# Optimization experiments

Measured on AMD Instinct MI355X. Metric: run time of the kernel, lower is better.

## Reference

```python
import jax, jax.numpy as jnp
import numpy as np

THRESH_FACTOR = 0.7


def ternarize(w):
    # w: [in_features, out_features]; per-row (dim 0) delta/alpha stats
    n = w.shape[1]
    abs_w = jnp.abs(w)
    delta = (THRESH_FACTOR / n) * abs_w.sum(axis=1, keepdims=True)  # [in, 1]
    mask = abs_w > delta
    count = mask.sum(axis=1, keepdims=True).astype(w.dtype)
    alpha = jnp.where(mask, abs_w, 0).sum(axis=1, keepdims=True) / count  # [in, 1]
    tern = jnp.where(w > delta, 1.0, jnp.where(w < -delta, -1.0, 0.0)).astype(w.dtype)
    return tern * alpha


def setup_inputs() -> dict:
    key = jax.random.key(0)
    k1, k2, k3 = jax.random.split(key, 3)
    B, IN, OUT = 8192, 4096, 4096
    x = jax.random.normal(k1, (B, IN), dtype=jnp.float32)
    # kaiming-uniform-ish then clamp to [-1, 1] as in the module
    bound_w = float(np.sqrt(6.0 / ((1.0 + 5.0) * IN)))
    weights = jax.random.uniform(k2, (IN, OUT), minval=-bound_w, maxval=bound_w, dtype=jnp.float32)
    weights = jnp.clip(weights, -1.0, 1.0)
    bound_b = 1.0 / float(np.sqrt(IN))
    bias = jax.random.uniform(k3, (OUT,), minval=-bound_b, maxval=bound_b, dtype=jnp.float32)
    return {"x": x, "weights": weights, "bias": bias}


def reference(x, weights, bias):
    w_t = ternarize(weights)
    return jnp.matmul(x, w_t) + bias
```

## Files before the change

### kernel.cpp

```cpp
#include <hip/hip_runtime.h>
#include <stdint.h>
#include <stddef.h>

#define IN_F 4096
#define OUT_F 4096

typedef int i32x4 __attribute__((ext_vector_type(4)));
typedef float f32x4 __attribute__((ext_vector_type(4)));


__device__ static inline void async16(const void* g, void* l) {
    __builtin_amdgcn_global_load_lds(
        (const __attribute__((address_space(1))) unsigned int*)g,
        (__attribute__((address_space(3))) unsigned int*)l,
        16, 0, 0);
}

__device__ static inline double wred_d(double v) {
#pragma unroll
    for (int o = 32; o > 0; o >>= 1) v += __shfl_down(v, o, 64);
    return v;
}

__device__ static inline int wred_i(int v) {
#pragma unroll
    for (int o = 32; o > 0; o >>= 1) v += __shfl_down(v, o, 64);
    return v;
}

__device__ static inline float wred_max(float v) {
#pragma unroll
    for (int o = 32; o > 0; o >>= 1) v = fmaxf(v, __shfl_down(v, o, 64));
    return v;
}


__global__ __launch_bounds__(256) void rowstats_tern_kernel(
    const float* __restrict__ w,
    float* __restrict__ alpha_o,
    int8_t* __restrict__ T) {
    __shared__ float rowbuf[OUT_F];
    __shared__ double sh_s[4], sh_m[4];
    __shared__ int sh_c[4];
    const int row = blockIdx.x;
    const int t = threadIdx.x;
    const int lane = t & 63, wv = t >> 6;
    const float4* wr = (const float4*)(w + (size_t)row * OUT_F);

    double s = 0.0;
#pragma unroll
    for (int it = 0; it < 4; ++it) {
        float4 v = wr[t + it * 256];
        ((float4*)rowbuf)[t + it * 256] = v;
        s += (double)fabsf(v.x) + (double)fabsf(v.y) +
             (double)fabsf(v.z) + (double)fabsf(v.w);
    }
    double sw = wred_d(s);
    if (lane == 0) sh_s[wv] = sw;
    __syncthreads();
    const double delta = (sh_s[0] + sh_s[1] + sh_s[2] + sh_s[3]) *
                         (0.7 / (double)OUT_F);

    int8_t* trow = T + (size_t)row * OUT_F;
    double ms = 0.0;
    int cnt = 0;
#pragma unroll
    for (int k = 0; k < 16; ++k) {
        float v = rowbuf[k * 256 + t];
        double a = (double)fabsf(v);
        if (a > delta) { ms += a; ++cnt; }
        int8_t q = 0;
        if ((double)v > delta)       q = 1;
        else if ((double)v < -delta) q = -1;
        trow[k * 256 + t] = q;
    }
    double msw = wred_d(ms);
    int cw = wred_i(cnt);
    if (lane == 0) { sh_m[wv] = msw; sh_c[wv] = cw; }
    __syncthreads();
    if (t == 0) {
        double mtot = sh_m[0] + sh_m[1] + sh_m[2] + sh_m[3];
        int ctot = sh_c[0] + sh_c[1] + sh_c[2] + sh_c[3];
        alpha_o[row] = (float)(mtot / (double)ctot);
    }
}


__global__ __launch_bounds__(256) void transpose_i8_kernel(
    const int8_t* __restrict__ T,
    int8_t* __restrict__ Tt) {
    __shared__ int8_t lds[64][72];
    const int t = threadIdx.x;
    const int i0 = blockIdx.y * 64;
    const int j0 = blockIdx.x * 64;

#pragma unroll
    for (int it = 0; it < 4; ++it) {
        int idx = it * 256 + t;
        int r = idx >> 4;
        int c4 = idx & 15;
        uchar4 v = *(const uchar4*)(T + (size_t)(i0 + r) * OUT_F + j0 + c4 * 4);
        lds[c4 * 4 + 0][r] = (int8_t)v.x;
        lds[c4 * 4 + 1][r] = (int8_t)v.y;
        lds[c4 * 4 + 2][r] = (int8_t)v.z;
        lds[c4 * 4 + 3][r] = (int8_t)v.w;
    }
    __syncthreads();
#pragma unroll
    for (int it = 0; it < 2; ++it) {
        int idx = it * 256 + t;
        int rr = idx >> 3;
        int cc = idx & 7;
        unsigned long long v = *(const unsigned long long*)&lds[rr][cc * 8];
        *(unsigned long long*)(Tt + (size_t)(j0 + rr) * IN_F + i0 + cc * 8) = v;
    }
}


__global__ __launch_bounds__(256) void xquant_kernel(
    const float* __restrict__ x,
    const float* __restrict__ alpha,
    int8_t* __restrict__ xq,
    float* __restrict__ scale_o) {
    __shared__ float rowbuf[IN_F];
    __shared__ float sh_mx[4];
    const int row = blockIdx.x;
    const int t = threadIdx.x;
    const int lane = t & 63, wv = t >> 6;
    const float4* xr = (const float4*)(x + (size_t)row * IN_F);
    const float4* ar = (const float4*)alpha;

    float mx = 0.0f;
#pragma unroll
    for (int it = 0; it < 4; ++it) {
        float4 v = xr[t + it * 256];
        float4 a = ar[t + it * 256];
        v.x *= a.x; v.y *= a.y; v.z *= a.z; v.w *= a.w;
        ((float4*)rowbuf)[t + it * 256] = v;
        mx = fmaxf(mx, fmaxf(fmaxf(fabsf(v.x), fabsf(v.y)),
                             fmaxf(fabsf(v.z), fabsf(v.w))));
    }
    float mw = wred_max(mx);
    if (lane == 0) sh_mx[wv] = mw;
    __syncthreads();
    const float rmax = fmaxf(fmaxf(sh_mx[0], sh_mx[1]), fmaxf(sh_mx[2], sh_mx[3]));
    const float inv = (rmax > 0.0f) ? (127.0f / rmax) : 0.0f;

    int8_t* qrow = xq + (size_t)row * IN_F;
#pragma unroll
    for (int k = 0; k < 16; ++k) {
        float v = rowbuf[k * 256 + t];
        qrow[k * 256 + t] = (int8_t)__float2int_rn(v * inv);
    }
    if (t == 0) scale_o[row] = (rmax > 0.0f) ? (rmax / 127.0f) : 1.0f;
}


#define GBARRIER() asm volatile("s_barrier" ::: "memory")

#define STAGE(G, GR0, TILE, LBASE, HALF)                                        \
    do {                                                                        \
        _Pragma("unroll")                                                       \
        for (int rr_ = 0; rr_ < 2; ++rr_) {                                     \
            const int L_ = (HALF) * 1024 + rr_ * 512 + t;                       \
            const int row_ = L_ >> 3;                                           \
            const int gch_ = (L_ & 7) ^ (row_ & 7);                             \
            async16((G) + (size_t)((GR0) + row_) * IN_F + (TILE) * 128 +        \
                        (gch_ << 4),                                            \
                    (LBASE) + (L_ << 4));                                       \
        }                                                                       \
    } while (0)

#define READ_A(BUF, MI0)                                                        \
    _Pragma("unroll")                                                           \
    for (int mi_ = 0; mi_ < 4; ++mi_) {                                         \
        a[2 * mi_]     = *(const i32x4*)((BUF) + offA_k0 + ((MI0) + mi_) * 2048); \
        a[2 * mi_ + 1] = *(const i32x4*)((BUF) + offA_k1 + ((MI0) + mi_) * 2048); \
    }

#define READ_B(BUF, NI0, DST)                                                   \
    _Pragma("unroll")                                                           \
    for (int ni_ = 0; ni_ < 2; ++ni_) {                                         \
        DST[2 * ni_]     = *(const i32x4*)((BUF) + offB_k0 + ((NI0) + ni_) * 2048); \
        DST[2 * ni_ + 1] = *(const i32x4*)((BUF) + offB_k1 + ((NI0) + ni_) * 2048); \
    }

#define MFMA_Q(MI0, NI0, BSRC)                                                  \
    do {                                                                        \
        __builtin_amdgcn_s_setprio(1);                                          \
        _Pragma("unroll")                                                       \
        for (int mi_ = 0; mi_ < 4; ++mi_) {                                     \
            _Pragma("unroll")                                                   \
            for (int ni_ = 0; ni_ < 2; ++ni_) {                                 \
                acc[(MI0) + mi_][(NI0) + ni_] =                                 \
                    __builtin_amdgcn_mfma_i32_16x16x64_i8(                      \
                        a[2 * mi_], BSRC[2 * ni_],                              \
                        acc[(MI0) + mi_][(NI0) + ni_], 0, 0, 0);                \
                acc[(MI0) + mi_][(NI0) + ni_] =                                 \
                    __builtin_amdgcn_mfma_i32_16x16x64_i8(                      \
                        a[2 * mi_ + 1], BSRC[2 * ni_ + 1],                      \
                        acc[(MI0) + mi_][(NI0) + ni_], 0, 0, 0);                \
            }                                                                   \
        }                                                                       \
        __builtin_amdgcn_s_setprio(0);                                          \
    } while (0)

__global__ __launch_bounds__(512, 2) void gemm_i8_8ph(
    const int8_t* __restrict__ Xq,
    const int8_t* __restrict__ Tq,
    const float* __restrict__ scale,
    const float* __restrict__ bias,
    float* __restrict__ out) {
    extern __shared__ __align__(16) int8_t lds[];
    const int K = IN_F;
    const int NT = K / 128;
    const int NI = NT / 2;

    const int t = threadIdx.x;
    const int lane = t & 63;
    const int wave = t >> 6;
    const int lm = lane & 15;
    const int qh = lane >> 4;
    const int wm = (wave >> 2) << 7;
    const int wn = (wave & 3) << 6;

    const int nwg = gridDim.x;
    const int id = blockIdx.x;
    const int swz = (id & 7) * (nwg >> 3) + (id >> 3);
    const int m0 = (swz >> 4) << 8;
    const int n0 = (swz & 15) << 8;

    int8_t* const A0  = lds;
    int8_t* const B0  = lds + 32768;
    int8_t* const A1b = lds + 65536;
    int8_t* const B1b = lds + 98304;

    const int swzs = lm & 7;
    const int offA_k0 = (wm + lm) * 128 + ((qh ^ swzs) << 4);
    const int offA_k1 = (wm + lm) * 128 + (((4 + qh) ^ swzs) << 4);
    const int offB_k0 = (wn + lm) * 128 + ((qh ^ swzs) << 4);
    const int offB_k1 = (wn + lm) * 128 + (((4 + qh) ^ swzs) << 4);

    i32x4 acc[8][4];
#pragma unroll
    for (int i = 0; i < 8; ++i)
#pragma unroll
        for (int j = 0; j < 4; ++j)
#pragma unroll
            for (int r = 0; r < 4; ++r) acc[i][j][r] = 0;

    i32x4 a[8], bA[4], bB[4];

    STAGE(Xq, m0, 0, A0, 0);
    STAGE(Xq, m0, 0, A0, 1);
    STAGE(Tq, n0, 0, B0, 0);
    STAGE(Tq, n0, 0, B0, 1);
    STAGE(Xq, m0, 1, A1b, 0);
    asm volatile("s_waitcnt vmcnt(2)" ::: "memory");
    GBARRIER();

#pragma unroll 1
    for (int i = 0; i < NI; ++i) {
        const int kt = 2 * i;
        READ_A(A0, 0);
        READ_B(B0, 0, bA);
        STAGE(Xq, m0, kt + 1, A1b, 1);
        GBARRIER();
        MFMA_Q(0, 0, bA);
        GBARRIER();
        READ_B(B0, 2, bB);
        STAGE(Tq, n0, kt + 1, B1b, 0);
        GBARRIER();
        MFMA_Q(0, 2, bB);
        GBARRIER();
        READ_A(A0, 4);
        STAGE(Tq, n0, kt + 1, B1b, 1);
        GBARRIER();
        MFMA_Q(4, 0, bA);
        GBARRIER();
        if (kt + 2 < NT) STAGE(Xq, m0, kt + 2, A0, 0);
        GBARRIER();
        MFMA_Q(4, 2, bB);
        if (i + 1 < NI) asm volatile("s_waitcnt vmcnt(2)" ::: "memory");
        else            asm volatile("s_waitcnt vmcnt(0)" ::: "memory");
        GBARRIER();
        READ_A(A1b, 0);
        READ_B(B1b, 0, bA);
        if (kt + 2 < NT) STAGE(Xq, m0, kt + 2, A0, 1);
        GBARRIER();
        MFMA_Q(0, 0, bA);
        GBARRIER();
        READ_B(B1b, 2, bB);
        if (kt + 2 < NT) STAGE(Tq, n0, kt + 2, B0, 0);
        GBARRIER();
        MFMA_Q(0, 2, bB);
        GBARRIER();
        READ_A(A1b, 4);
        if (kt + 2 < NT) STAGE(Tq, n0, kt + 2, B0, 1);
        GBARRIER();
        MFMA_Q(4, 0, bA);
        GBARRIER();
        if (kt + 3 < NT) STAGE(Xq, m0, kt + 3, A1b, 0);
        GBARRIER();
        MFMA_Q(4, 2, bB);
        if (i + 1 < NI) asm volatile("s_waitcnt vmcnt(2)" ::: "memory");
        GBARRIER();
    }

    const int q4 = qh << 2;
#pragma unroll
    for (int mi = 0; mi < 8; ++mi) {
        float sc[4];
#pragma unroll
        for (int r = 0; r < 4; ++r) sc[r] = scale[m0 + wm + mi * 16 + q4 + r];
#pragma unroll
        for (int ni = 0; ni < 4; ++ni) {
            int col = n0 + wn + ni * 16 + lm;
            float b = bias[col];
#pragma unroll
            for (int r = 0; r < 4; ++r) {
                int row = m0 + wm + mi * 16 + q4 + r;
                out[(size_t)row * OUT_F + col] =
                    (float)acc[mi][ni][r] * sc[r] + b;
            }
        }
    }
}


extern "C" void kernel_launch(void* const* d_in, const int* in_sizes, int n_in,
                              void* d_out, int out_size, void* d_ws, size_t ws_size,
                              hipStream_t stream) {
    const float* x = (const float*)d_in[0];
    const float* w = (const float*)d_in[1];
    const float* bias = (const float*)d_in[2];
    float* out = (float*)d_out;
    const int B = in_sizes[0] / IN_F;

    char* ws = (char*)d_ws;
    int8_t* Tt = (int8_t*)ws;
    int8_t* T = (int8_t*)(ws + (size_t)16777216);
    int8_t* Xq = (int8_t*)(ws + (size_t)16777216);
    float* alpha = (float*)(ws + (size_t)50331648);
    float* scale = (float*)(ws + (size_t)50331648 + 16384);

    static int lds_set = 0;
    if (!lds_set) {
        hipFuncSetAttribute((const void*)gemm_i8_8ph,
                            hipFuncAttributeMaxDynamicSharedMemorySize, 131072);
        lds_set = 1;
    }

    rowstats_tern_kernel<<<IN_F, 256, 0, stream>>>(w, alpha, T);
    transpose_i8_kernel<<<dim3(OUT_F / 64, IN_F / 64), 256, 0, stream>>>(T, Tt);
    xquant_kernel<<<B, 256, 0, stream>>>(x, alpha, Xq, scale);
    const int nwg = (B / 256) * (OUT_F / 256);
    gemm_i8_8ph<<<dim3(nwg), dim3(512), 131072, stream>>>(Xq, Tt, scale, bias, out);
}
```

Before: 384.9 us.

## Fuse ternarization into transpose, register-stage quantization, reorder GEMM prefetch

Row statistics now only compute alpha and delta, and ternarization moves into the transpose kernel, which reads fp32 weights directly and writes packed int8 transposed tiles. This removes the intermediate int8 weight matrix. The activation quantizer keeps each thread's 16 values in registers and writes one 16-byte packed store instead of staging through LDS. The GEMM main loop issues B-tile prefetches earlier and waits with a deeper vmcnt. The trade-off is that the weights are read twice, and delta shares a workspace slot with scale, which relies on kernel ordering.

```diff
diff --git a/kernel.cpp b/kernel.cpp
--- a/kernel.cpp
+++ b/kernel.cpp
@@ -6,7 +6,6 @@
 #define OUT_F 4096
 
 typedef int i32x4 __attribute__((ext_vector_type(4)));
-typedef float f32x4 __attribute__((ext_vector_type(4)));
 
 
 __device__ static inline void async16(const void* g, void* l) {
@@ -35,25 +34,24 @@
 }
 
 
-__global__ __launch_bounds__(256) void rowstats_tern_kernel(
+__global__ __launch_bounds__(256) void rowstats_kernel(
     const float* __restrict__ w,
     float* __restrict__ alpha_o,
-    int8_t* __restrict__ T) {
-    __shared__ float rowbuf[OUT_F];
+    double* __restrict__ delta_o) {
     __shared__ double sh_s[4], sh_m[4];
     __shared__ int sh_c[4];
     const int row = blockIdx.x;
     const int t = threadIdx.x;
     const int lane = t & 63, wv = t >> 6;
-    const float4* wr = (const float4*)(w + (size_t)row * OUT_F);
-
+    const float4* wr = (const float4*)(w + (size_t)row * OUT_F + t * 16);
+
+    float4 v[4];
     double s = 0.0;
 #pragma unroll
-    for (int it = 0; it < 4; ++it) {
-        float4 v = wr[t + it * 256];
-        ((float4*)rowbuf)[t + it * 256] = v;
-        s += (double)fabsf(v.x) + (double)fabsf(v.y) +
-             (double)fabsf(v.z) + (double)fabsf(v.w);
+    for (int i = 0; i < 4; ++i) {
+        v[i] = wr[i];
+        s += (double)fabsf(v[i].x) + (double)fabsf(v[i].y) +
+             (double)fabsf(v[i].z) + (double)fabsf(v[i].w);
     }
     double sw = wred_d(s);
     if (lane == 0) sh_s[wv] = sw;
@@ -61,18 +59,16 @@
     const double delta = (sh_s[0] + sh_s[1] + sh_s[2] + sh_s[3]) *
                          (0.7 / (double)OUT_F);
 
-    int8_t* trow = T + (size_t)row * OUT_F;
     double ms = 0.0;
     int cnt = 0;
 #pragma unroll
-    for (int k = 0; k < 16; ++k) {
-        float v = rowbuf[k * 256 + t];
-        double a = (double)fabsf(v);
-        if (a > delta) { ms += a; ++cnt; }
-        int8_t q = 0;
-        if ((double)v > delta)       q = 1;
-        else if ((double)v < -delta) q = -1;
-        trow[k * 256 + t] = q;
+    for (int i = 0; i < 4; ++i) {
+        float f[4] = {v[i].x, v[i].y, v[i].z, v[i].w};
+#pragma unroll
+        for (int j = 0; j < 4; ++j) {
+            double a = (double)fabsf(f[j]);
+            if (a > delta) { ms += a; ++cnt; }
+        }
     }
     double msw = wred_d(ms);
     int cw = wred_i(cnt);
@@ -82,37 +78,54 @@
         double mtot = sh_m[0] + sh_m[1] + sh_m[2] + sh_m[3];
         int ctot = sh_c[0] + sh_c[1] + sh_c[2] + sh_c[3];
         alpha_o[row] = (float)(mtot / (double)ctot);
-    }
-}
-
-
-__global__ __launch_bounds__(256) void transpose_i8_kernel(
-    const int8_t* __restrict__ T,
+        delta_o[row] = delta;
+    }
+}
+
+
+__global__ __launch_bounds__(256) void tern_transpose_kernel(
+    const float* __restrict__ w,
+    const double* __restrict__ delta_i,
     int8_t* __restrict__ Tt) {
-    __shared__ int8_t lds[64][72];
+    __shared__ unsigned int ldsb[128 * 33];
     const int t = threadIdx.x;
-    const int i0 = blockIdx.y * 64;
-    const int j0 = blockIdx.x * 64;
-
+    const int i0 = blockIdx.y * 128;
+    const int j0 = blockIdx.x * 128;
+
+#pragma unroll
+    for (int it = 0; it < 4; ++it) {
+        int bb = it * 256 + t;
+        int rg = bb >> 5;
+        int cc = bb & 31;
+        unsigned int col[4] = {0u, 0u, 0u, 0u};
+#pragma unroll
+        for (int k = 0; k < 4; ++k) {
+            int irow = i0 + rg * 4 + k;
+            float4 v = *(const float4*)(w + (size_t)irow * OUT_F + j0 + cc * 4);
+            double d = delta_i[irow];
+            float f[4] = {v.x, v.y, v.z, v.w};
+#pragma unroll
+            for (int j = 0; j < 4; ++j) {
+                int q = ((double)f[j] > d) ? 1 : (((double)f[j] < -d) ? -1 : 0);
+                col[j] |= (unsigned int)(q & 0xff) << (k * 8);
+            }
+        }
+#pragma unroll
+        for (int j = 0; j < 4; ++j)
+            ldsb[(cc * 4 + j) * 33 + rg] = col[j];
+    }
+    __syncthreads();
 #pragma unroll
     for (int it = 0; it < 4; ++it) {
         int idx = it * 256 + t;
-        int r = idx >> 4;
-        int c4 = idx & 15;
-        uchar4 v = *(const uchar4*)(T + (size_t)(i0 + r) * OUT_F + j0 + c4 * 4);
-        lds[c4 * 4 + 0][r] = (int8_t)v.x;
-        lds[c4 * 4 + 1][r] = (int8_t)v.y;
-        lds[c4 * 4 + 2][r] = (int8_t)v.z;
-        lds[c4 * 4 + 3][r] = (int8_t)v.w;
-    }
-    __syncthreads();
-#pragma unroll
-    for (int it = 0; it < 2; ++it) {
-        int idx = it * 256 + t;
         int rr = idx >> 3;
-        int cc = idx & 7;
-        unsigned long long v = *(const unsigned long long*)&lds[rr][cc * 8];
-        *(unsigned long long*)(Tt + (size_t)(j0 + rr) * IN_F + i0 + cc * 8) = v;
+        int c2 = idx & 7;
+        uint4 o;
+        o.x = ldsb[rr * 33 + c2 * 4 + 0];
+        o.y = ldsb[rr * 33 + c2 * 4 + 1];
+        o.z = ldsb[rr * 33 + c2 * 4 + 2];
+        o.w = ldsb[rr * 33 + c2 * 4 + 3];
+        *(uint4*)(Tt + (size_t)(j0 + rr) * IN_F + i0 + c2 * 16) = o;
     }
 }
 
@@ -122,21 +135,21 @@
     const float* __restrict__ alpha,
     int8_t* __restrict__ xq,
     float* __restrict__ scale_o) {
-    __shared__ float rowbuf[IN_F];
     __shared__ float sh_mx[4];
     const int row = blockIdx.x;
     const int t = threadIdx.x;
     const int lane = t & 63, wv = t >> 6;
-    const float4* xr = (const float4*)(x + (size_t)row * IN_F);
-    const float4* ar = (const float4*)alpha;
-
+    const float4* xr = (const float4*)(x + (size_t)row * IN_F + t * 16);
+    const float4* ar = (const float4*)(alpha + t * 16);
+
+    float4 xs[4];
     float mx = 0.0f;
 #pragma unroll
-    for (int it = 0; it < 4; ++it) {
-        float4 v = xr[t + it * 256];
-        float4 a = ar[t + it * 256];
+    for (int i = 0; i < 4; ++i) {
+        float4 v = xr[i];
+        float4 a = ar[i];
         v.x *= a.x; v.y *= a.y; v.z *= a.z; v.w *= a.w;
-        ((float4*)rowbuf)[t + it * 256] = v;
+        xs[i] = v;
         mx = fmaxf(mx, fmaxf(fmaxf(fabsf(v.x), fabsf(v.y)),
                              fmaxf(fabsf(v.z), fabsf(v.w))));
     }
@@ -146,12 +159,20 @@
     const float rmax = fmaxf(fmaxf(sh_mx[0], sh_mx[1]), fmaxf(sh_mx[2], sh_mx[3]));
     const float inv = (rmax > 0.0f) ? (127.0f / rmax) : 0.0f;
 
-    int8_t* qrow = xq + (size_t)row * IN_F;
-#pragma unroll
-    for (int k = 0; k < 16; ++k) {
-        float v = rowbuf[k * 256 + t];
-        qrow[k * 256 + t] = (int8_t)__float2int_rn(v * inv);
-    }
+    uint4 o;
+    unsigned int* op = (unsigned int*)&o;
+#pragma unroll
+    for (int i = 0; i < 4; ++i) {
+        float f[4] = {xs[i].x, xs[i].y, xs[i].z, xs[i].w};
+        unsigned int d = 0;
+#pragma unroll
+        for (int j = 0; j < 4; ++j) {
+            int q = __float2int_rn(f[j] * inv);
+            d |= (unsigned int)(q & 0xff) << (j * 8);
+        }
+        op[i] = d;
+    }
+    *(uint4*)(xq + (size_t)row * IN_F + t * 16) = o;
     if (t == 0) scale_o[row] = (rmax > 0.0f) ? (rmax / 127.0f) : 1.0f;
 }
 
@@ -255,8 +276,9 @@
     STAGE(Xq, m0, 0, A0, 1);
     STAGE(Tq, n0, 0, B0, 0);
     STAGE(Tq, n0, 0, B0, 1);
+    STAGE(Tq, n0, 1, B1b, 0);
     STAGE(Xq, m0, 1, A1b, 0);
-    asm volatile("s_waitcnt vmcnt(2)" ::: "memory");
+    asm volatile("s_waitcnt vmcnt(4)" ::: "memory");
     GBARRIER();
 
 #pragma unroll 1
@@ -264,46 +286,46 @@
         const int kt = 2 * i;
         READ_A(A0, 0);
         READ_B(B0, 0, bA);
+        STAGE(Tq, n0, kt + 1, B1b, 1);
+        GBARRIER();
+        MFMA_Q(0, 0, bA);
+        GBARRIER();
+        READ_B(B0, 2, bB);
         STAGE(Xq, m0, kt + 1, A1b, 1);
         GBARRIER();
-        MFMA_Q(0, 0, bA);
-        GBARRIER();
-        READ_B(B0, 2, bB);
-        STAGE(Tq, n0, kt + 1, B1b, 0);
-        GBARRIER();
         MFMA_Q(0, 2, bB);
         GBARRIER();
         READ_A(A0, 4);
-        STAGE(Tq, n0, kt + 1, B1b, 1);
+        if (kt + 2 < NT) STAGE(Tq, n0, kt + 2, B0, 0);
         GBARRIER();
         MFMA_Q(4, 0, bA);
         GBARRIER();
         if (kt + 2 < NT) STAGE(Xq, m0, kt + 2, A0, 0);
         GBARRIER();
         MFMA_Q(4, 2, bB);
-        if (i + 1 < NI) asm volatile("s_waitcnt vmcnt(2)" ::: "memory");
+        if (i + 1 < NI) asm volatile("s_waitcnt vmcnt(4)" ::: "memory");
         else            asm volatile("s_waitcnt vmcnt(0)" ::: "memory");
         GBARRIER();
         READ_A(A1b, 0);
         READ_B(B1b, 0, bA);
+        if (kt + 2 < NT) STAGE(Tq, n0, kt + 2, B0, 1);
+        GBARRIER();
+        MFMA_Q(0, 0, bA);
+        GBARRIER();
+        READ_B(B1b, 2, bB);
         if (kt + 2 < NT) STAGE(Xq, m0, kt + 2, A0, 1);
         GBARRIER();
-        MFMA_Q(0, 0, bA);
-        GBARRIER();
-        READ_B(B1b, 2, bB);
-        if (kt + 2 < NT) STAGE(Tq, n0, kt + 2, B0, 0);
-        GBARRIER();
         MFMA_Q(0, 2, bB);
         GBARRIER();
         READ_A(A1b, 4);
-        if (kt + 2 < NT) STAGE(Tq, n0, kt + 2, B0, 1);
+        if (kt + 3 < NT) STAGE(Tq, n0, kt + 3, B1b, 0);
         GBARRIER();
         MFMA_Q(4, 0, bA);
         GBARRIER();
         if (kt + 3 < NT) STAGE(Xq, m0, kt + 3, A1b, 0);
         GBARRIER();
         MFMA_Q(4, 2, bB);
-        if (i + 1 < NI) asm volatile("s_waitcnt vmcnt(2)" ::: "memory");
+        if (i + 1 < NI) asm volatile("s_waitcnt vmcnt(4)" ::: "memory");
         GBARRIER();
     }
 
@@ -339,9 +361,9 @@
 
     char* ws = (char*)d_ws;
     int8_t* Tt = (int8_t*)ws;
-    int8_t* T = (int8_t*)(ws + (size_t)16777216);
     int8_t* Xq = (int8_t*)(ws + (size_t)16777216);
     float* alpha = (float*)(ws + (size_t)50331648);
+    double* delta = (double*)(ws + (size_t)50331648 + 16384);
     float* scale = (float*)(ws + (size_t)50331648 + 16384);
 
     static int lds_set = 0;
@@ -351,8 +373,8 @@
         lds_set = 1;
     }
 
-    rowstats_tern_kernel<<<IN_F, 256, 0, stream>>>(w, alpha, T);
-    transpose_i8_kernel<<<dim3(OUT_F / 64, IN_F / 64), 256, 0, stream>>>(T, Tt);
+    rowstats_kernel<<<IN_F, 256, 0, stream>>>(w, alpha, delta);
+    tern_transpose_kernel<<<dim3(OUT_F / 128, IN_F / 128), 256, 0, stream>>>(w, delta, Tt);
     xquant_kernel<<<B, 256, 0, stream>>>(x, alpha, Xq, scale);
     const int nwg = (B / 256) * (OUT_F / 256);
     gemm_i8_8ph<<<dim3(nwg), dim3(512), 131072, stream>>>(Xq, Tt, scale, bias, out);
```

Measured after the change: 390.9 us. Within noise of the previous version (+1.6%).
